# Performance work log

Hardware: AMD Instinct MI355X
Metric: run time of the kernel (lower is better)

## Reference

```python
import jax, jax.numpy as jnp
import numpy as np

B, S, D, H = 2, 2048, 512, 8
DK = D // H


def setup_inputs() -> dict:
    key = jax.random.key(0)
    ks = jax.random.split(key, 6)
    q = jax.random.normal(ks[0], (B, S, D), dtype=jnp.float32)
    k = jax.random.normal(ks[1], (B, S, D), dtype=jnp.float32)
    v = jax.random.normal(ks[2], (B, S, D), dtype=jnp.float32)
    mask = jax.random.randint(ks[3], (1, 1, S, S), 0, 2, dtype=jnp.int32)
    # nn.Linear weights [out, in]; scaled like torch default init
    Wq = jax.random.normal(ks[4], (D, D), dtype=jnp.float32) / np.sqrt(D)
    Wo = jax.random.normal(ks[5], (D, D), dtype=jnp.float32) / np.sqrt(D)
    return {"q": q, "k": k, "v": v, "mask": mask, "Wq": Wq, "Wo": Wo}


def _split_heads(x):
    # [B,S,D] -> [B,H,S,DK]
    return x.reshape(B, S, H, DK).transpose(0, 2, 1, 3)


def reference(q, k, v, mask, Wq, Wo):
    # NOTE: original module applies Wq to q, k AND v (faithful to source bug)
    query = _split_heads(q @ Wq.T)
    key_ = _split_heads(k @ Wq.T)
    value = _split_heads(v @ Wq.T)
    scores = jnp.einsum("bhqd,bhkd->bhqk", query, key_) / np.sqrt(DK).astype(np.float32)
    # original uses masked_fill_(mask==0, 1e-09) BEFORE softmax (not -inf)
    scores = jnp.where(mask == 0, jnp.float32(1e-9), scores)
    attn = jax.nn.softmax(scores, axis=-1)  # dropout p=0.0 -> identity
    x = jnp.einsum("bhqk,bhkd->bhqd", attn, value)
    x = x.transpose(0, 2, 1, 3).reshape(B, S, D)
    return x @ Wo.T
```

## Files before the change

### kernel.cpp

```cpp
#include <hip/hip_runtime.h>
#include <hip/hip_bf16.h>
#include <stdint.h>

#define S_LEN 2048
#define D_MOD 512
#define N_H   8
#define D_K   64

typedef short v8s __attribute__((ext_vector_type(8)));
typedef short v4s __attribute__((ext_vector_type(4)));
typedef float v4f __attribute__((ext_vector_type(4)));

__device__ __forceinline__ short f2bf(float f) {
  union { float f; unsigned u; } a; a.f = f;
  unsigned u = a.u;
  u += 0x7fffu + ((u >> 16) & 1u);
  return (short)(u >> 16);
}
__device__ __forceinline__ short f2bfh(float f) {
  union { float f; unsigned u; } a; a.f = f;
  return (short)((a.u + 0x8000u) >> 16);
}
__device__ __forceinline__ float bf2f(short s) {
  union { unsigned u; float f; } x;
  x.u = ((unsigned)(unsigned short)s) << 16;
  return x.f;
}

__device__ __forceinline__ v4f mfma16(v8s a, v8s b, v4f c) {
  return __builtin_amdgcn_mfma_f32_16x16x32_bf16(a, b, c, 0, 0, 0);
}
__device__ __forceinline__ v4f mfma16x16(v4s a, v4s b, v4f c) {
  return __builtin_amdgcn_mfma_f32_16x16x16bf16_1k(a, b, c, 0, 0, 0);
}

__global__ __launch_bounds__(256) void proj_kernel(
    const float* __restrict__ q, const float* __restrict__ k,
    const float* __restrict__ v, const float* __restrict__ Wq,
    const float* __restrict__ Wo, const int* __restrict__ mask,
    short* __restrict__ QP, short* __restrict__ KP, short* __restrict__ VT,
    short* __restrict__ Wob, unsigned long long* __restrict__ mp)
{
  const int z = blockIdx.z;
  const int tid = threadIdx.x;
  if (z == 3) {
    int bid = blockIdx.x * 8 + blockIdx.y;
    if (bid < 256) {
      int id = bid * 256 + tid;
      const int4* m4 = (const int4*)(mask + (size_t)id * 64);
      unsigned long long w = 0ull;
#pragma unroll
      for (int j = 0; j < 16; j++) {
        int4 mv = m4[j];
        w |= (unsigned long long)(mv.x != 0) << (j * 4 + 0);
        w |= (unsigned long long)(mv.y != 0) << (j * 4 + 1);
        w |= (unsigned long long)(mv.z != 0) << (j * 4 + 2);
        w |= (unsigned long long)(mv.w != 0) << (j * 4 + 3);
      }
      mp[id] = w;
    } else {
      unsigned off = (bid - 256) * 256 + tid;
      float4 x = ((const float4*)Wo)[off];
      v4s p; p.x = f2bf(x.x); p.y = f2bf(x.y); p.z = f2bf(x.z); p.w = f2bf(x.w);
      ((v4s*)Wob)[off] = p;
    }
    return;
  }
  const float* __restrict__ A = (z == 0) ? q : ((z == 1) ? k : v);
  const int m0 = blockIdx.x * 64, n0 = blockIdx.y * 64;
  const int wave = tid >> 6, lane = tid & 63;
  const int quad = lane >> 4, l15 = lane & 15;
  const int wm = wave >> 1, wn = wave & 1;
  __shared__ short As[64][72];
  __shared__ short Bs[64][72];
  v4f acc[2][2];
#pragma unroll
  for (int i = 0; i < 2; i++)
#pragma unroll
    for (int j = 0; j < 2; j++) acc[i][j] = (v4f){0.f, 0.f, 0.f, 0.f};

  float4 a4[4], b4[4];
#pragma unroll
  for (int i = 0; i < 4; i++) {
    int fi = tid + i * 256, r = fi >> 4, c = (fi & 15) << 2;
    a4[i] = *(const float4*)&A[(m0 + r) * 512 + c];
    b4[i] = *(const float4*)&Wq[(n0 + r) * 512 + c];
  }

  for (int kk = 0; kk < 512; kk += 64) {
    __syncthreads();
#pragma unroll
    for (int i = 0; i < 4; i++) {
      int fi = tid + i * 256, r = fi >> 4, c = (fi & 15) << 2;
      v4s ap; ap.x = f2bf(a4[i].x); ap.y = f2bf(a4[i].y); ap.z = f2bf(a4[i].z); ap.w = f2bf(a4[i].w);
      *(v4s*)&As[r][c] = ap;
      v4s bp; bp.x = f2bf(b4[i].x); bp.y = f2bf(b4[i].y); bp.z = f2bf(b4[i].z); bp.w = f2bf(b4[i].w);
      *(v4s*)&Bs[r][c] = bp;
    }
    __syncthreads();
    if (kk + 64 < 512) {
#pragma unroll
      for (int i = 0; i < 4; i++) {
        int fi = tid + i * 256, r = fi >> 4, c = (fi & 15) << 2;
        a4[i] = *(const float4*)&A[(m0 + r) * 512 + kk + 64 + c];
        b4[i] = *(const float4*)&Wq[(n0 + r) * 512 + kk + 64 + c];
      }
    }
#pragma unroll
    for (int ms = 0; ms < 2; ms++)
#pragma unroll
      for (int ns = 0; ns < 2; ns++)
#pragma unroll
        for (int ks = 0; ks < 2; ks++) {
          union { v8s v; v4s h2[2]; } a, bb;
          a.h2[0]  = *(const v4s*)&As[wm * 32 + ms * 16 + l15][ks * 32 + quad * 8];
          a.h2[1]  = *(const v4s*)&As[wm * 32 + ms * 16 + l15][ks * 32 + quad * 8 + 4];
          bb.h2[0] = *(const v4s*)&Bs[wn * 32 + ns * 16 + l15][ks * 32 + quad * 8];
          bb.h2[1] = *(const v4s*)&Bs[wn * 32 + ns * 16 + l15][ks * 32 + quad * 8 + 4];
          acc[ms][ns] = mfma16(a.v, bb.v, acc[ms][ns]);
        }
  }
#pragma unroll
  for (int ms = 0; ms < 2; ms++)
#pragma unroll
    for (int ns = 0; ns < 2; ns++) {
      int mb = m0 + wm * 32 + ms * 16 + quad * 4;
      int n  = n0 + wn * 32 + ns * 16 + l15;
      int bI = mb >> 11, s = mb & 2047, hh = n >> 6, dk = n & 63;
      if (z == 2) {
        v4s pv;
        pv.x = f2bf(acc[ms][ns][0]); pv.y = f2bf(acc[ms][ns][1]);
        pv.z = f2bf(acc[ms][ns][2]); pv.w = f2bf(acc[ms][ns][3]);
        *(v4s*)&VT[((bI * N_H + hh) * D_K + dk) * S_LEN + s] = pv;
      } else {
        short* dst = (z == 0) ? QP : KP;
#pragma unroll
        for (int r = 0; r < 4; r++)
          dst[((bI * N_H + hh) * S_LEN + (s + r)) * D_K + dk] = f2bf(acc[ms][ns][r]);
      }
    }
}

__global__ __launch_bounds__(256, 4) void attn_kernel(
    const short* __restrict__ QP, const short* __restrict__ KP,
    const short* __restrict__ VT, const unsigned long long* __restrict__ MP,
    short* __restrict__ XB, float* __restrict__ LP)
{
  const int bx = blockIdx.x;
  const int qt = bx & 31, qu = bx >> 5;
  const int h = blockIdx.y, b = blockIdx.z;
  const int tid = threadIdx.x;
  const int wave = tid >> 6, lane = tid & 63;
  const int quad = lane >> 4, l15 = lane & 15;
  const short* Qh = QP + ((b * N_H + h) * S_LEN) * D_K;
  const short* Kh = KP + ((b * N_H + h) * S_LEN) * D_K;
  const short* Vh = VT + ((b * N_H + h) * D_K) * S_LEN;

  __shared__ short Ks[64][72];
  __shared__ short Vs[64][72];

  const int qrow = qt * 64 + wave * 16;
  const int srow = tid >> 2;
  const int sc   = (tid & 3) * 16;
  const int ck0  = qu * 512;

  v8s aQ[2];
#pragma unroll
  for (int ks = 0; ks < 2; ks++)
    aQ[ks] = *(const v8s*)&Qh[(qrow + l15) * D_K + ks * 32 + quad * 8];

  const float C1 = 0.18033688011112042f;
  const float C2 = -11.541560327111707f;
  const v4s ONES4 = {16256, 16256, 16256, 16256};
  v4f accX[4], accL = (v4f){0.f, 0.f, 0.f, 0.f};
#pragma unroll
  for (int u = 0; u < 4; u++) accX[u] = (v4f){0.f, 0.f, 0.f, 0.f};

  v8s kr[2], vr[2];
#pragma unroll
  for (int j = 0; j < 2; j++) {
    kr[j] = *(const v8s*)&Kh[(ck0 + srow) * D_K + sc + j * 8];
    vr[j] = *(const v8s*)&Vh[srow * S_LEN + ck0 + sc + j * 8];
  }
  unsigned long long mwc = MP[(qrow + l15) * 32 + qu * 8];
  unsigned long long mwn = 0ull;

  for (int kt = 0; kt < 8; kt++) {
    __syncthreads();
#pragma unroll
    for (int j = 0; j < 2; j++) {
      *(v8s*)&Ks[srow][sc + j * 8] = kr[j];
      *(v8s*)&Vs[srow][sc + j * 8] = vr[j];
    }
    __syncthreads();

    if (kt + 1 < 8) {
      const int c1 = ck0 + (kt + 1) * 64;
#pragma unroll
      for (int j = 0; j < 2; j++) {
        kr[j] = *(const v8s*)&Kh[(c1 + srow) * D_K + sc + j * 8];
        vr[j] = *(const v8s*)&Vh[srow * S_LEN + c1 + sc + j * 8];
      }
      mwn = MP[(qrow + l15) * 32 + qu * 8 + kt + 1];
    }

    v4s pa[4];
#pragma unroll
    for (int tp = 0; tp < 4; tp++) {
      v8s bK0 = *(const v8s*)&Ks[tp * 16 + l15][quad * 8];
      v8s bK1 = *(const v8s*)&Ks[tp * 16 + l15][32 + quad * 8];
      v4f s = mfma16(bK0, aQ[0], (v4f){0.f, 0.f, 0.f, 0.f});
      s = mfma16(bK1, aQ[1], s);
      unsigned mb = (unsigned)(mwc >> (tp * 16 + quad * 4));
      v4s pk;
#pragma unroll
      for (int r = 0; r < 4; r++) {
        float se = ((mb >> r) & 1u) ? s[r] : 0.0f;
        float p = __builtin_amdgcn_exp2f(fmaf(se, C1, C2));
        pk[r] = f2bfh(p);
      }
      pa[tp] = pk;
    }

#pragma unroll
    for (int u = 0; u < 4; u++) {
      const short* vb_ = &Vs[u * 16 + l15][quad * 4];
#pragma unroll
      for (int tp = 0; tp < 4; tp++) {
        v4s bV = *(const v4s*)&vb_[tp * 16];
        accX[u] = mfma16x16(pa[tp], bV, accX[u]);
      }
    }
#pragma unroll
    for (int tp = 0; tp < 4; tp++)
      accL = mfma16x16(pa[tp], ONES4, accL);

    mwc = mwn;
  }

  short* xq = XB + (size_t)qu * 2097152u;
#pragma unroll
  for (int u = 0; u < 4; u++)
#pragma unroll
    for (int r = 0; r < 4; r++) {
      int srw = qrow + quad * 4 + r;
      xq[(b * S_LEN + srw) * D_MOD + h * D_K + u * 16 + l15] = f2bf(accX[u][r]);
    }
  if (l15 == 0) {
#pragma unroll
    for (int r = 0; r < 4; r++) {
      int srw = qrow + quad * 4 + r;
      LP[((qu * 2 + b) * S_LEN + srw) * N_H + h] = accL[r];
    }
  }
}

__global__ __launch_bounds__(256) void outproj_kernel(
    const short* __restrict__ XB, const float* __restrict__ LP,
    const short* __restrict__ Wob, float* __restrict__ out)
{
  const int m0 = blockIdx.x * 64, n0 = blockIdx.y * 64;
  const int tid = threadIdx.x;
  const int wave = tid >> 6, lane = tid & 63;
  const int quad = lane >> 4, l15 = lane & 15;
  const int wm = wave >> 1, wn = wave & 1;
  __shared__ short As[64][72];
  __shared__ short Bs[64][72];
  __shared__ float Linv[64][8];

#pragma unroll
  for (int i = 0; i < 2; i++) {
    int e = tid + i * 256;
    int rr = e >> 3, hh = e & 7;
    int s = m0 + rr, bb = s >> 11, sl = s & 2047;
    float l = 0.f;
#pragma unroll
    for (int qu = 0; qu < 4; qu++)
      l += LP[((qu * 2 + bb) * S_LEN + sl) * N_H + hh];
    Linv[rr][hh] = 1.0f / l;
  }

  v4f acc[2][2];
#pragma unroll
  for (int i = 0; i < 2; i++)
#pragma unroll
    for (int j = 0; j < 2; j++) acc[i][j] = (v4f){0.f, 0.f, 0.f, 0.f};

  float af[2][8];
  v8s b8[2];
#pragma unroll
  for (int i = 0; i < 2; i++) {
    int fi = tid + i * 256, r = fi >> 3, c = (fi & 7) << 3;
    size_t base = (size_t)(m0 + r) * 512 + c;
#pragma unroll
    for (int j = 0; j < 8; j++) af[i][j] = 0.f;
#pragma unroll
    for (int qu = 0; qu < 4; qu++) {
      v8s t = *(const v8s*)(XB + (size_t)qu * 2097152u + base);
#pragma unroll
      for (int j = 0; j < 8; j++) af[i][j] += bf2f(t[j]);
    }
    b8[i] = *(const v8s*)&Wob[(n0 + r) * 512 + c];
  }
  __syncthreads();

  for (int kk = 0; kk < 512; kk += 64) {
#pragma unroll
    for (int i = 0; i < 2; i++) {
      int fi = tid + i * 256, r = fi >> 3, c = (fi & 7) << 3;
      float inv = Linv[r][kk >> 6];
      v8s ap;
#pragma unroll
      for (int j = 0; j < 8; j++) ap[j] = f2bf(af[i][j] * inv);
      *(v8s*)&As[r][c] = ap;
      *(v8s*)&Bs[r][c] = b8[i];
    }
    __syncthreads();
    if (kk + 64 < 512) {
#pragma unroll
      for (int i = 0; i < 2; i++) {
        int fi = tid + i * 256, r = fi >> 3, c = (fi & 7) << 3;
        size_t base = (size_t)(m0 + r) * 512 + kk + 64 + c;
#pragma unroll
        for (int j = 0; j < 8; j++) af[i][j] = 0.f;
#pragma unroll
        for (int qu = 0; qu < 4; qu++) {
          v8s t = *(const v8s*)(XB + (size_t)qu * 2097152u + base);
#pragma unroll
          for (int j = 0; j < 8; j++) af[i][j] += bf2f(t[j]);
        }
        b8[i] = *(const v8s*)&Wob[(n0 + r) * 512 + kk + 64 + c];
      }
    }
#pragma unroll
    for (int ms = 0; ms < 2; ms++)
#pragma unroll
      for (int ns = 0; ns < 2; ns++)
#pragma unroll
        for (int ks = 0; ks < 2; ks++) {
          union { v8s v; v4s h2[2]; } a, bb;
          a.h2[0]  = *(const v4s*)&As[wm * 32 + ms * 16 + l15][ks * 32 + quad * 8];
          a.h2[1]  = *(const v4s*)&As[wm * 32 + ms * 16 + l15][ks * 32 + quad * 8 + 4];
          bb.h2[0] = *(const v4s*)&Bs[wn * 32 + ns * 16 + l15][ks * 32 + quad * 8];
          bb.h2[1] = *(const v4s*)&Bs[wn * 32 + ns * 16 + l15][ks * 32 + quad * 8 + 4];
          acc[ms][ns] = mfma16(a.v, bb.v, acc[ms][ns]);
        }
    __syncthreads();
  }
#pragma unroll
  for (int ms = 0; ms < 2; ms++)
#pragma unroll
    for (int ns = 0; ns < 2; ns++) {
      int n = n0 + wn * 32 + ns * 16 + l15;
#pragma unroll
      for (int r = 0; r < 4; r++) {
        int m = m0 + wm * 32 + ms * 16 + quad * 4 + r;
        out[m * 512 + n] = acc[ms][ns][r];
      }
    }
}

extern "C" void kernel_launch(void* const* d_in, const int* in_sizes, int n_in,
                              void* d_out, int out_size, void* d_ws, size_t ws_size,
                              hipStream_t stream) {
  const float* q  = (const float*)d_in[0];
  const float* k  = (const float*)d_in[1];
  const float* v  = (const float*)d_in[2];
  const int* mask = (const int*)d_in[3];
  const float* Wq = (const float*)d_in[4];
  const float* Wo = (const float*)d_in[5];
  float* out = (float*)d_out;
  char* ws = (char*)d_ws;
  short* QP = (short*)(ws);
  short* KP = (short*)(ws + (4u << 20));
  short* VT = (short*)(ws + (8u << 20));
  unsigned long long* MP = (unsigned long long*)(ws + (16u << 20));
  short* Wob = (short*)(ws + (16u << 20) + (512u << 10));
  short* XB = (short*)(ws + (17u << 20));
  float* LP = (float*)(ws + (33u << 20));

  proj_kernel<<<dim3(64, 8, 4), 256, 0, stream>>>(q, k, v, Wq, Wo, mask,
                                                  QP, KP, VT, Wob, MP);
  attn_kernel<<<dim3(128, N_H, 2), 256, 0, stream>>>(QP, KP, VT, MP, XB, LP);
  outproj_kernel<<<dim3(64, 8, 1), 256, 0, stream>>>(XB, LP, Wob, out);
}
```

Before: 155.7 us.

## Double-buffer K/V tiles in LDS and use 512-thread attention blocks

The attention kernel now uses 8 waves per block covering 128 query rows, so each K/V tile staged in LDS serves twice as many queries. K/V tiles are double-buffered in shared memory, which cuts the per-iteration barriers from two to one and lets the next tile's store overlap with the current tile's compute. In exchange the grid is half as large, LDS use per block doubles, and the launch bound of 512 threads with 4 blocks may press on registers.

Measured after the change: 151.7 us. 2.5% less time.

```diff
diff --git a/kernel.cpp b/kernel.cpp
--- a/kernel.cpp
+++ b/kernel.cpp
@@ -141,13 +141,13 @@
     }
 }
 
-__global__ __launch_bounds__(256, 4) void attn_kernel(
+__global__ __launch_bounds__(512, 4) void attn_kernel(
     const short* __restrict__ QP, const short* __restrict__ KP,
     const short* __restrict__ VT, const unsigned long long* __restrict__ MP,
     short* __restrict__ XB, float* __restrict__ LP)
 {
   const int bx = blockIdx.x;
-  const int qt = bx & 31, qu = bx >> 5;
+  const int qt = bx & 15, qu = bx >> 4;
   const int h = blockIdx.y, b = blockIdx.z;
   const int tid = threadIdx.x;
   const int wave = tid >> 6, lane = tid & 63;
@@ -156,12 +156,12 @@
   const short* Kh = KP + ((b * N_H + h) * S_LEN) * D_K;
   const short* Vh = VT + ((b * N_H + h) * D_K) * S_LEN;
 
-  __shared__ short Ks[64][72];
-  __shared__ short Vs[64][72];
-
-  const int qrow = qt * 64 + wave * 16;
-  const int srow = tid >> 2;
-  const int sc   = (tid & 3) * 16;
+  __shared__ short Ks[2][64][72];
+  __shared__ short Vs[2][64][72];
+
+  const int qrow = qt * 128 + wave * 16;
+  const int srow = tid >> 3;
+  const int sc   = (tid & 7) * 8;
   const int ck0  = qu * 512;
 
   v8s aQ[2];
@@ -176,39 +176,28 @@
 #pragma unroll
   for (int u = 0; u < 4; u++) accX[u] = (v4f){0.f, 0.f, 0.f, 0.f};
 
-  v8s kr[2], vr[2];
-#pragma unroll
-  for (int j = 0; j < 2; j++) {
-    kr[j] = *(const v8s*)&Kh[(ck0 + srow) * D_K + sc + j * 8];
-    vr[j] = *(const v8s*)&Vh[srow * S_LEN + ck0 + sc + j * 8];
-  }
+  v8s kr = *(const v8s*)&Kh[(ck0 + srow) * D_K + sc];
+  v8s vr = *(const v8s*)&Vh[srow * S_LEN + ck0 + sc];
+  *(v8s*)&Ks[0][srow][sc] = kr;
+  *(v8s*)&Vs[0][srow][sc] = vr;
   unsigned long long mwc = MP[(qrow + l15) * 32 + qu * 8];
   unsigned long long mwn = 0ull;
+  __syncthreads();
 
   for (int kt = 0; kt < 8; kt++) {
-    __syncthreads();
-#pragma unroll
-    for (int j = 0; j < 2; j++) {
-      *(v8s*)&Ks[srow][sc + j * 8] = kr[j];
-      *(v8s*)&Vs[srow][sc + j * 8] = vr[j];
-    }
-    __syncthreads();
-
+    const int cur = kt & 1;
     if (kt + 1 < 8) {
       const int c1 = ck0 + (kt + 1) * 64;
-#pragma unroll
-      for (int j = 0; j < 2; j++) {
-        kr[j] = *(const v8s*)&Kh[(c1 + srow) * D_K + sc + j * 8];
-        vr[j] = *(const v8s*)&Vh[srow * S_LEN + c1 + sc + j * 8];
-      }
+      kr = *(const v8s*)&Kh[(c1 + srow) * D_K + sc];
+      vr = *(const v8s*)&Vh[srow * S_LEN + c1 + sc];
       mwn = MP[(qrow + l15) * 32 + qu * 8 + kt + 1];
     }
 
     v4s pa[4];
 #pragma unroll
     for (int tp = 0; tp < 4; tp++) {
-      v8s bK0 = *(const v8s*)&Ks[tp * 16 + l15][quad * 8];
-      v8s bK1 = *(const v8s*)&Ks[tp * 16 + l15][32 + quad * 8];
+      v8s bK0 = *(const v8s*)&Ks[cur][tp * 16 + l15][quad * 8];
+      v8s bK1 = *(const v8s*)&Ks[cur][tp * 16 + l15][32 + quad * 8];
       v4f s = mfma16(bK0, aQ[0], (v4f){0.f, 0.f, 0.f, 0.f});
       s = mfma16(bK1, aQ[1], s);
       unsigned mb = (unsigned)(mwc >> (tp * 16 + quad * 4));
@@ -224,7 +213,7 @@
 
 #pragma unroll
     for (int u = 0; u < 4; u++) {
-      const short* vb_ = &Vs[u * 16 + l15][quad * 4];
+      const short* vb_ = &Vs[cur][u * 16 + l15][quad * 4];
 #pragma unroll
       for (int tp = 0; tp < 4; tp++) {
         v4s bV = *(const v4s*)&vb_[tp * 16];
@@ -235,6 +224,11 @@
     for (int tp = 0; tp < 4; tp++)
       accL = mfma16x16(pa[tp], ONES4, accL);
 
+    if (kt + 1 < 8) {
+      *(v8s*)&Ks[cur ^ 1][srow][sc] = kr;
+      *(v8s*)&Vs[cur ^ 1][srow][sc] = vr;
+    }
+    __syncthreads();
     mwc = mwn;
   }
 
@@ -381,6 +375,6 @@
 
   proj_kernel<<<dim3(64, 8, 4), 256, 0, stream>>>(q, k, v, Wq, Wo, mask,
                                                   QP, KP, VT, Wob, MP);
-  attn_kernel<<<dim3(128, N_H, 2), 256, 0, stream>>>(QP, KP, VT, MP, XB, LP);
+  attn_kernel<<<dim3(64, N_H, 2), 512, 0, stream>>>(QP, KP, VT, MP, XB, LP);
   outproj_kernel<<<dim3(64, 8, 1), 256, 0, stream>>>(XB, LP, Wob, out);
 }
```
